# Kernel tuning notes

Hardware: AMD Instinct MI355X
Metric: run time of the kernel (lower is better)

## Reference

```python
import jax, jax.numpy as jnp
import numpy as np

N, D = 16384, 256
T = 0.5
C = 100


def setup_inputs() -> dict:
    key = jax.random.key(0)
    x = jax.random.normal(key, (N, D), dtype=jnp.float32)
    # L2-normalize rows (standard for contrastive embeddings; also keeps
    # exp(sim/T) in fp32 range, matching the module's intended use)
    x = x / jnp.linalg.norm(x, axis=1, keepdims=True)
    return {"x": x}


def reference(x) -> jnp.ndarray:
    # sim[i,j] = <x_i, x_j> / T ; loss = (1/C) * sum_i log(sum_j exp(sim[i,j]))
    sim = jnp.exp(jnp.matmul(x, x.T) / T)          # [N, N]
    row = jnp.log(jnp.sum(sim, axis=1))            # [N]
    return jnp.sum(row) / C                        # scalar
```

## Files before the change

kernel.cpp:

```cpp
#include <hip/hip_runtime.h>
#include <hip/hip_bf16.h>
#include <math.h>


#define N_ROWS 16384
#define KD     256
#define NBAND  32
#define FI_TOTAL 4224
#define NBLK   256
#define NSLOT  96

#define SCALE_SQRT 1.6986436f

typedef short short8 __attribute__((ext_vector_type(8)));
typedef float f32x4  __attribute__((ext_vector_type(4)));

typedef __attribute__((address_space(3))) void       lds_void;
typedef const __attribute__((address_space(1))) void gm_void;

__device__ __forceinline__ float fast_exp2(float x) {
#if __has_builtin(__builtin_amdgcn_exp2f)
    return __builtin_amdgcn_exp2f(x);
#else
    return exp2f(x);
#endif
}

__device__ __forceinline__ void gll16(const void* g, void* l) {
    __builtin_amdgcn_global_load_lds((gm_void*)g, (lds_void*)l, 16, 0, 0);
}

__global__ void convert_kernel(const float* __restrict__ x, unsigned short* __restrict__ xb,
                               float* __restrict__ rowacc, float* __restrict__ out) {
    const int bx = blockIdx.x, tid = threadIdx.x;
    if (bx < (NSLOT * N_ROWS) / 1024)
        *(float4*)(rowacc + (size_t)(bx * 256 + tid) * 4) = (float4){0.f, 0.f, 0.f, 0.f};
    if (bx == 2000 && tid == 0) out[0] = 0.f;
    int i = (bx * 256 + tid) * 4;
    float4 v = *(const float4*)(x + i);
    ushort4 o;
    {
        unsigned int u;
        u = __float_as_uint(v.x * SCALE_SQRT); u += 0x7fff + ((u >> 16) & 1); o.x = (unsigned short)(u >> 16);
        u = __float_as_uint(v.y * SCALE_SQRT); u += 0x7fff + ((u >> 16) & 1); o.y = (unsigned short)(u >> 16);
        u = __float_as_uint(v.z * SCALE_SQRT); u += 0x7fff + ((u >> 16) & 1); o.z = (unsigned short)(u >> 16);
        u = __float_as_uint(v.w * SCALE_SQRT); u += 0x7fff + ((u >> 16) & 1); o.w = (unsigned short)(u >> 16);
    }
    *(ushort4*)(xb + i) = o;
}

__global__ __launch_bounds__(512, 2)
void simloss_main(const unsigned short* __restrict__ xb, float* __restrict__ rowacc) {
    __shared__ __align__(128) char smem[4 * 32768 + 2048 + 4096];
    float* const rowred = (float*)(smem + 131072);
    float* const colred = (float*)(smem + 131072 + 2048);

    const int tid  = threadIdx.x;
    const int lane = tid & 63;
    const int w    = tid >> 6;
    const int l15  = lane & 15;
    const int lg   = lane >> 4;
    const int b    = blockIdx.x;

    int f          = (b * 33) >> 1;
    const int fEnd = ((b + 1) * 33) >> 1;
    const int rowSlot = 64 + (b & 31);

    int rb = (int)((sqrtf((float)f + 1.f) - 1.f) * 0.5f);
    while (4 * (rb + 1) * (rb + 2) <= f) ++rb;
    while (4 * rb * (rb + 1) > f) --rb;

    #pragma unroll 1
    while (f < fEnd) {
        while (4 * (rb + 1) * (rb + 2) <= f) ++rb;
        const int bandStart = 4 * rb * (rb + 1);
        const int cblk0   = f - bandStart;
        const int bandEnd = bandStart + 8 * (rb + 1);
        const int lim = fEnd < bandEnd ? fEnd : bandEnd;
        const int NI  = lim - f;
        const int r0  = rb * 512;

        auto stageB = [&](int buf, int cblk) {
            if (cblk > 255) cblk = 255;
            #pragma unroll
            for (int g = 0; g < 4; ++g) {
                const int fr = w * 4 + g;
                const int ct = fr >> 3, kt = fr & 7;
                const unsigned short* s =
                    xb + (size_t)(cblk * 64 + ct * 16 + l15) * KD + kt * 32 + lg * 8;
                gll16(s, smem + buf * 32768 + fr * 1024);
            }
        };
        stageB(0, cblk0);
        stageB(1, cblk0 + 1);

        short8 afrag[4][8];
        #pragma unroll
        for (int m = 0; m < 4; ++m) {
            const unsigned short* ar = xb + (size_t)(r0 + w * 64 + m * 16 + l15) * KD + lg * 8;
            #pragma unroll
            for (int kt = 0; kt < 8; ++kt)
                afrag[m][kt] = *(const short8*)(ar + kt * 32);
        }
        #pragma unroll
        for (int m = 0; m < 4; ++m)
            #pragma unroll
            for (int kt = 0; kt < 8; ++kt)
                asm volatile("" : "+v"(afrag[m][kt]));

        float rowsum[4][4] = {{0.f}};

        #pragma unroll 1
        for (int fi = 0; fi < NI; ++fi) {
            if (fi + 2 < NI) {
                stageB((fi + 2) & 3, cblk0 + fi + 2);
                asm volatile("s_waitcnt vmcnt(8)" ::: "memory");
            } else if (fi + 1 < NI) {
                asm volatile("s_waitcnt vmcnt(4)" ::: "memory");
            } else {
                asm volatile("s_waitcnt vmcnt(0)" ::: "memory");
            }
            asm volatile("s_waitcnt lgkmcnt(0)" ::: "memory");
            __builtin_amdgcn_s_barrier();
            asm volatile("" ::: "memory");

            if (fi > 0 && tid < 64) {
                const int pc = cblk0 + fi - 1;
                if (pc < rb * 8) {
                    const float* cp = colred + ((fi - 1) & 1) * 512;
                    float cs = 0.f;
                    #pragma unroll
                    for (int w2 = 0; w2 < 8; ++w2) cs += cp[w2 * 64 + tid];
                    rowacc[(size_t)rb * N_ROWS + pc * 64 + tid] = cs;
                }
            }

            const char* bbase = smem + (fi & 3) * 32768;
            float* cw = colred + (fi & 1) * 512;
            #pragma unroll
            for (int ct = 0; ct < 4; ++ct) {
                short8 bfrag[8];
                #pragma unroll
                for (int kt = 0; kt < 8; ++kt)
                    bfrag[kt] = *(const short8*)(bbase + (ct * 8 + kt) * 1024 + lane * 16);
                f32x4 acc[4];
                #pragma unroll
                for (int m = 0; m < 4; ++m) acc[m] = (f32x4){0.f, 0.f, 0.f, 0.f};
                #pragma unroll
                for (int kt = 0; kt < 8; ++kt)
                    #pragma unroll
                    for (int m = 0; m < 4; ++m)
                        acc[m] = __builtin_amdgcn_mfma_f32_16x16x32_bf16(afrag[m][kt], bfrag[kt], acc[m], 0, 0, 0);
                float csum = 0.f;
                #pragma unroll
                for (int m = 0; m < 4; ++m)
                    #pragma unroll
                    for (int r = 0; r < 4; ++r) {
                        float e = fast_exp2(acc[m][r]);
                        rowsum[m][r] += e;
                        csum += e;
                    }
                csum += __shfl_xor(csum, 16);
                csum += __shfl_xor(csum, 32);
                if (lg == 0) cw[w * 64 + ct * 16 + l15] = csum;
            }
            asm volatile("" ::: "memory");
        }

        __syncthreads();

        if (tid < 64) {
            const int pc = cblk0 + NI - 1;
            if (pc < rb * 8) {
                const float* cp = colred + ((NI - 1) & 1) * 512;
                float cs = 0.f;
                #pragma unroll
                for (int w2 = 0; w2 < 8; ++w2) cs += cp[w2 * 64 + tid];
                rowacc[(size_t)rb * N_ROWS + pc * 64 + tid] = cs;
            }
        }

        #pragma unroll
        for (int m = 0; m < 4; ++m)
            #pragma unroll
            for (int r = 0; r < 4; ++r) {
                float v = rowsum[m][r];
                v += __shfl_xor(v, 1);
                v += __shfl_xor(v, 2);
                v += __shfl_xor(v, 4);
                v += __shfl_xor(v, 8);
                if (l15 == 0) rowred[w * 64 + m * 16 + lg * 4 + r] = v;
            }
        __syncthreads();
        rowacc[(size_t)rowSlot * N_ROWS + r0 + tid] = rowred[tid];

        f = lim;
    }
}

__global__ void finalize_kernel(const float* __restrict__ rowacc, float* __restrict__ out) {
    int i = blockIdx.x * 256 + threadIdx.x;
    float s = 0.f;
    #pragma unroll 8
    for (int k = 0; k < NSLOT; ++k) s += rowacc[(size_t)k * N_ROWS + i];
    float v = logf(s);
    #pragma unroll
    for (int off = 1; off < 64; off <<= 1) v += __shfl_xor(v, off);
    __shared__ float red[4];
    if ((threadIdx.x & 63) == 0) red[threadIdx.x >> 6] = v;
    __syncthreads();
    if (threadIdx.x == 0)
        atomicAdd(out, (red[0] + red[1] + red[2] + red[3]) * 0.01f);
}

extern "C" void kernel_launch(void* const* d_in, const int* in_sizes, int n_in,
                              void* d_out, int out_size, void* d_ws, size_t ws_size,
                              hipStream_t stream) {
    const float* x = (const float*)d_in[0];
    unsigned short* xb = (unsigned short*)d_ws;
    float* rowacc = (float*)((char*)d_ws + (size_t)N_ROWS * KD * 2);
    float* out = (float*)d_out;

    convert_kernel<<<(N_ROWS * KD) / (256 * 4), 256, 0, stream>>>(x, xb, rowacc, out);
    simloss_main<<<NBLK, 512, 0, stream>>>(xb, rowacc);
    finalize_kernel<<<N_ROWS / 256, 256, 0, stream>>>(rowacc, out);
}
```

Baseline: 149.9 us.

## Interleave B-tile prefetch per sub-tile with barriers and MFMA priority

Splits the staging of the next-next B tile into four per-sub-tile issues spread across the inner ct loop, so global-to-LDS loads interleave with MFMA work instead of being issued in a burst. It adds block barriers around each sub-tile, raises wave priority during the MFMA section, and splits the column-sum accumulation into four independent chains to shorten the dependency chain. The per-sub-tile barriers add synchronization overhead in exchange for finer-grained overlap. It also drops the clamp on the column block index and guards the second prefetch with NI>1.

```diff
diff --git a/kernel.cpp b/kernel.cpp
--- a/kernel.cpp
+++ b/kernel.cpp
@@ -5,8 +5,6 @@
 
 #define N_ROWS 16384
 #define KD     256
-#define NBAND  32
-#define FI_TOTAL 4224
 #define NBLK   256
 #define NSLOT  96
 
@@ -80,19 +78,20 @@
         const int NI  = lim - f;
         const int r0  = rb * 512;
 
-        auto stageB = [&](int buf, int cblk) {
-            if (cblk > 255) cblk = 255;
-            #pragma unroll
-            for (int g = 0; g < 4; ++g) {
-                const int fr = w * 4 + g;
-                const int ct = fr >> 3, kt = fr & 7;
-                const unsigned short* s =
-                    xb + (size_t)(cblk * 64 + ct * 16 + l15) * KD + kt * 32 + lg * 8;
-                gll16(s, smem + buf * 32768 + fr * 1024);
-            }
+        auto stageG = [&](int buf, int cblk, int g) {
+            const int fr = w * 4 + g;
+            const int ct = fr >> 3, kt = fr & 7;
+            const unsigned short* s =
+                xb + (size_t)(cblk * 64 + ct * 16 + l15) * KD + kt * 32 + lg * 8;
+            gll16(s, smem + buf * 32768 + fr * 1024);
         };
-        stageB(0, cblk0);
-        stageB(1, cblk0 + 1);
+
+        #pragma unroll
+        for (int g = 0; g < 4; ++g) stageG(0, cblk0, g);
+        if (NI > 1) {
+            #pragma unroll
+            for (int g = 0; g < 4; ++g) stageG(1, cblk0 + 1, g);
+        }
 
         short8 afrag[4][8];
         #pragma unroll
@@ -108,41 +107,42 @@
             for (int kt = 0; kt < 8; ++kt)
                 asm volatile("" : "+v"(afrag[m][kt]));
 
+        asm volatile("s_waitcnt vmcnt(0)" ::: "memory");
+        __builtin_amdgcn_s_barrier();
+
         float rowsum[4][4] = {{0.f}};
 
         #pragma unroll 1
         for (int fi = 0; fi < NI; ++fi) {
-            if (fi + 2 < NI) {
-                stageB((fi + 2) & 3, cblk0 + fi + 2);
-                asm volatile("s_waitcnt vmcnt(8)" ::: "memory");
-            } else if (fi + 1 < NI) {
-                asm volatile("s_waitcnt vmcnt(4)" ::: "memory");
-            } else {
-                asm volatile("s_waitcnt vmcnt(0)" ::: "memory");
-            }
-            asm volatile("s_waitcnt lgkmcnt(0)" ::: "memory");
-            __builtin_amdgcn_s_barrier();
-            asm volatile("" ::: "memory");
-
-            if (fi > 0 && tid < 64) {
-                const int pc = cblk0 + fi - 1;
-                if (pc < rb * 8) {
-                    const float* cp = colred + ((fi - 1) & 1) * 512;
-                    float cs = 0.f;
-                    #pragma unroll
-                    for (int w2 = 0; w2 < 8; ++w2) cs += cp[w2 * 64 + tid];
-                    rowacc[(size_t)rb * N_ROWS + pc * 64 + tid] = cs;
-                }
-            }
-
             const char* bbase = smem + (fi & 3) * 32768;
             float* cw = colred + (fi & 1) * 512;
-            #pragma unroll
-            for (int ct = 0; ct < 4; ++ct) {
+
+            #pragma unroll
+            for (int p = 0; p < 4; ++p) {
                 short8 bfrag[8];
                 #pragma unroll
                 for (int kt = 0; kt < 8; ++kt)
-                    bfrag[kt] = *(const short8*)(bbase + (ct * 8 + kt) * 1024 + lane * 16);
+                    bfrag[kt] = *(const short8*)(bbase + (p * 8 + kt) * 1024 + lane * 16);
+                if (fi + 2 < NI) stageG((fi + 2) & 3, cblk0 + fi + 2, p);
+                if (p == 0 && fi > 0 && tid < 64) {
+                    const int pc = cblk0 + fi - 1;
+                    if (pc < rb * 8) {
+                        const float* cp = colred + ((fi - 1) & 1) * 512;
+                        float cs = 0.f;
+                        #pragma unroll
+                        for (int w2 = 0; w2 < 8; ++w2) cs += cp[w2 * 64 + tid];
+                        rowacc[(size_t)rb * N_ROWS + pc * 64 + tid] = cs;
+                    }
+                }
+                if (p == 3) {
+                    if (fi + 2 < NI) { asm volatile("s_waitcnt vmcnt(4)" ::: "memory"); }
+                    else             { asm volatile("s_waitcnt vmcnt(0)" ::: "memory"); }
+                }
+                __builtin_amdgcn_sched_barrier(0);
+                __builtin_amdgcn_s_barrier();
+                __builtin_amdgcn_sched_barrier(0);
+
+                __builtin_amdgcn_s_setprio(1);
                 f32x4 acc[4];
                 #pragma unroll
                 for (int m = 0; m < 4; ++m) acc[m] = (f32x4){0.f, 0.f, 0.f, 0.f};
@@ -151,20 +151,25 @@
                     #pragma unroll
                     for (int m = 0; m < 4; ++m)
                         acc[m] = __builtin_amdgcn_mfma_f32_16x16x32_bf16(afrag[m][kt], bfrag[kt], acc[m], 0, 0, 0);
-                float csum = 0.f;
-                #pragma unroll
-                for (int m = 0; m < 4; ++m)
-                    #pragma unroll
-                    for (int r = 0; r < 4; ++r) {
-                        float e = fast_exp2(acc[m][r]);
-                        rowsum[m][r] += e;
-                        csum += e;
-                    }
+                __builtin_amdgcn_s_setprio(0);
+
+                float c0 = 0.f, c1 = 0.f, c2 = 0.f, c3 = 0.f;
+                #pragma unroll
+                for (int m = 0; m < 4; ++m) {
+                    float e0 = fast_exp2(acc[m][0]); rowsum[m][0] += e0; c0 += e0;
+                    float e1 = fast_exp2(acc[m][1]); rowsum[m][1] += e1; c1 += e1;
+                    float e2 = fast_exp2(acc[m][2]); rowsum[m][2] += e2; c2 += e2;
+                    float e3 = fast_exp2(acc[m][3]); rowsum[m][3] += e3; c3 += e3;
+                }
+                float csum = (c0 + c1) + (c2 + c3);
                 csum += __shfl_xor(csum, 16);
                 csum += __shfl_xor(csum, 32);
-                if (lg == 0) cw[w * 64 + ct * 16 + l15] = csum;
+                if (lg == 0) cw[w * 64 + p * 16 + l15] = csum;
+
+                asm volatile("s_waitcnt lgkmcnt(0)" ::: "memory");
+                __builtin_amdgcn_sched_barrier(0);
+                __builtin_amdgcn_s_barrier();
             }
-            asm volatile("" ::: "memory");
         }
 
         __syncthreads();
```

Result: slower. 169.8 us (+13.2%).

## Software-pipeline exp epilogue of previous column tile behind next tile's MFMAs

Applied to the files above, without the earlier changes.

Restructures the per-fragment inner loop into four phases with ping-pong accumulators, so the exp2 and row/column-sum work for one 16-column tile runs while the MFMAs for the next tile are issued. The B-fragment LDS loads are split into two halves to reduce register pressure. Column-reduction buffers move from double to triple buffering, and the cross-wave column sum is written out two iterations later. The change adds accumulator registers (risking spills at 2 waves per SIMD) and more complex tail handling, and it drops the clamp on cblk.

```diff
diff --git a/kernel.cpp b/kernel.cpp
--- a/kernel.cpp
+++ b/kernel.cpp
@@ -5,8 +5,6 @@
 
 #define N_ROWS 16384
 #define KD     256
-#define NBAND  32
-#define FI_TOTAL 4224
 #define NBLK   256
 #define NSLOT  96
 
@@ -49,9 +47,49 @@
     *(ushort4*)(xb + i) = o;
 }
 
+#define PROC_PREV(ACCP, CWP, PSLOT)                                            \
+  {                                                                            \
+    float c0 = 0.f, c1 = 0.f, c2 = 0.f, c3 = 0.f;                              \
+    _Pragma("unroll")                                                          \
+    for (int m = 0; m < 4; ++m) {                                              \
+      float e0 = fast_exp2(ACCP[m][0]); rowsum[m][0] += e0; c0 += e0;          \
+      float e1 = fast_exp2(ACCP[m][1]); rowsum[m][1] += e1; c1 += e1;          \
+      float e2 = fast_exp2(ACCP[m][2]); rowsum[m][2] += e2; c2 += e2;          \
+      float e3 = fast_exp2(ACCP[m][3]); rowsum[m][3] += e3; c3 += e3;          \
+    }                                                                          \
+    float csum_ = (c0 + c1) + (c2 + c3);                                       \
+    csum_ += __shfl_xor(csum_, 16);                                            \
+    csum_ += __shfl_xor(csum_, 32);                                            \
+    if (lg == 0) (CWP)[w * 64 + (PSLOT) * 16 + l15] = csum_;                   \
+  }
+
+#define PHASE(P, ACCC, ACCP, PSLOT, CWP, DOPREV)                               \
+  {                                                                            \
+    short8 bfA[4], bfB[4];                                                     \
+    _Pragma("unroll")                                                          \
+    for (int kt = 0; kt < 4; ++kt)                                             \
+      bfA[kt] = *(const short8*)(bbase + ((P) * 8 + kt) * 1024 + lane * 16);   \
+    _Pragma("unroll")                                                          \
+    for (int m = 0; m < 4; ++m) ACCC[m] = (f32x4){0.f, 0.f, 0.f, 0.f};         \
+    _Pragma("unroll")                                                          \
+    for (int kt = 0; kt < 4; ++kt)                                             \
+      _Pragma("unroll")                                                        \
+      for (int m = 0; m < 4; ++m)                                              \
+        ACCC[m] = __builtin_amdgcn_mfma_f32_16x16x32_bf16(afrag[m][kt], bfA[kt], ACCC[m], 0, 0, 0); \
+    _Pragma("unroll")                                                          \
+    for (int kt = 0; kt < 4; ++kt)                                             \
+      bfB[kt] = *(const short8*)(bbase + ((P) * 8 + 4 + kt) * 1024 + lane * 16); \
+    _Pragma("unroll")                                                          \
+    for (int kt = 0; kt < 4; ++kt)                                             \
+      _Pragma("unroll")                                                        \
+      for (int m = 0; m < 4; ++m)                                              \
+        ACCC[m] = __builtin_amdgcn_mfma_f32_16x16x32_bf16(afrag[m][4 + kt], bfB[kt], ACCC[m], 0, 0, 0); \
+    if (DOPREV) PROC_PREV(ACCP, CWP, PSLOT)                                    \
+  }
+
 __global__ __launch_bounds__(512, 2)
 void simloss_main(const unsigned short* __restrict__ xb, float* __restrict__ rowacc) {
-    __shared__ __align__(128) char smem[4 * 32768 + 2048 + 4096];
+    __shared__ __align__(128) char smem[4 * 32768 + 2048 + 3 * 2048];
     float* const rowred = (float*)(smem + 131072);
     float* const colred = (float*)(smem + 131072 + 2048);
 
@@ -81,7 +119,6 @@
         const int r0  = rb * 512;
 
         auto stageB = [&](int buf, int cblk) {
-            if (cblk > 255) cblk = 255;
             #pragma unroll
             for (int g = 0; g < 4; ++g) {
                 const int fr = w * 4 + g;
@@ -92,7 +129,7 @@
             }
         };
         stageB(0, cblk0);
-        stageB(1, cblk0 + 1);
+        if (NI > 1) stageB(1, cblk0 + 1);
 
         short8 afrag[4][8];
         #pragma unroll
@@ -109,6 +146,7 @@
                 asm volatile("" : "+v"(afrag[m][kt]));
 
         float rowsum[4][4] = {{0.f}};
+        f32x4 accA[4], accB[4];
 
         #pragma unroll 1
         for (int fi = 0; fi < NI; ++fi) {
@@ -124,10 +162,10 @@
             __builtin_amdgcn_s_barrier();
             asm volatile("" ::: "memory");
 
-            if (fi > 0 && tid < 64) {
-                const int pc = cblk0 + fi - 1;
+            if (fi >= 2 && tid < 64) {
+                const int pc = cblk0 + fi - 2;
                 if (pc < rb * 8) {
-                    const float* cp = colred + ((fi - 1) & 1) * 512;
+                    const float* cp = colred + ((fi - 2) % 3) * 512;
                     float cs = 0.f;
                     #pragma unroll
                     for (int w2 = 0; w2 < 8; ++w2) cs += cp[w2 * 64 + tid];
@@ -136,47 +174,39 @@
             }
 
             const char* bbase = smem + (fi & 3) * 32768;
-            float* cw = colred + (fi & 1) * 512;
-            #pragma unroll
-            for (int ct = 0; ct < 4; ++ct) {
-                short8 bfrag[8];
-                #pragma unroll
-                for (int kt = 0; kt < 8; ++kt)
-                    bfrag[kt] = *(const short8*)(bbase + (ct * 8 + kt) * 1024 + lane * 16);
-                f32x4 acc[4];
-                #pragma unroll
-                for (int m = 0; m < 4; ++m) acc[m] = (f32x4){0.f, 0.f, 0.f, 0.f};
-                #pragma unroll
-                for (int kt = 0; kt < 8; ++kt)
-                    #pragma unroll
-                    for (int m = 0; m < 4; ++m)
-                        acc[m] = __builtin_amdgcn_mfma_f32_16x16x32_bf16(afrag[m][kt], bfrag[kt], acc[m], 0, 0, 0);
-                float csum = 0.f;
-                #pragma unroll
-                for (int m = 0; m < 4; ++m)
-                    #pragma unroll
-                    for (int r = 0; r < 4; ++r) {
-                        float e = fast_exp2(acc[m][r]);
-                        rowsum[m][r] += e;
-                        csum += e;
-                    }
-                csum += __shfl_xor(csum, 16);
-                csum += __shfl_xor(csum, 32);
-                if (lg == 0) cw[w * 64 + ct * 16 + l15] = csum;
-            }
+            float* cwCur  = colred + (fi % 3) * 512;
+            float* cwPrev = colred + ((fi + 2) % 3) * 512;
+
+            PHASE(0, accA, accB, 3, cwPrev, (fi > 0))
+            PHASE(1, accB, accA, 0, cwCur, 1)
+            PHASE(2, accA, accB, 1, cwCur, 1)
+            PHASE(3, accB, accA, 2, cwCur, 1)
             asm volatile("" ::: "memory");
         }
 
+        PROC_PREV(accB, colred + ((NI - 1) % 3) * 512, 3)
         __syncthreads();
 
         if (tid < 64) {
-            const int pc = cblk0 + NI - 1;
-            if (pc < rb * 8) {
-                const float* cp = colred + ((NI - 1) & 1) * 512;
-                float cs = 0.f;
-                #pragma unroll
-                for (int w2 = 0; w2 < 8; ++w2) cs += cp[w2 * 64 + tid];
-                rowacc[(size_t)rb * N_ROWS + pc * 64 + tid] = cs;
+            if (NI >= 2) {
+                const int pc = cblk0 + NI - 2;
+                if (pc < rb * 8) {
+                    const float* cp = colred + ((NI - 2) % 3) * 512;
+                    float cs = 0.f;
+                    #pragma unroll
+                    for (int w2 = 0; w2 < 8; ++w2) cs += cp[w2 * 64 + tid];
+                    rowacc[(size_t)rb * N_ROWS + pc * 64 + tid] = cs;
+                }
+            }
+            {
+                const int pc = cblk0 + NI - 1;
+                if (pc < rb * 8) {
+                    const float* cp = colred + ((NI - 1) % 3) * 512;
+                    float cs = 0.f;
+                    #pragma unroll
+                    for (int w2 = 0; w2 < 8; ++w2) cs += cp[w2 * 64 + tid];
+                    rowacc[(size_t)rb * N_ROWS + pc * 64 + tid] = cs;
+                }
             }
         }
 
```

Result: slower. 155.6 us (+3.8%).
